# Performance work log

Hardware: AMD Instinct MI355X
Metric: run time of the kernel (lower is better)

Reference implementation:

```python
import jax, jax.numpy as jnp
import numpy as np

SR = 44100
D = SR * 30          # duration_samples = 1_323_000
N = 1024             # number of note events
L = 32768            # max note length in samples
W = 1024             # hann window length (module's window_length)
H = 8                # harmonics in the synth
K = 128              # FIR taps in the effect chain
LAT = 2              # time_latent_size


def setup_inputs() -> dict:
    key = jax.random.key(0)
    ks = jax.random.split(key, 10)
    freq_rad = jax.random.uniform(ks[0], (N,), jnp.float32, 0.01, 0.3)
    velocity = jax.random.uniform(ks[1], (N,), jnp.float32, 1.0, 127.0)
    starts = jax.random.randint(ks[2], (N,), 0, D - L, dtype=jnp.int32)
    lengths = jax.random.randint(ks[3], (N,), 2048, L + 1, dtype=jnp.int32)
    # time_embedder: Linear(1,32) -> ReLU -> Linear(32,LAT)
    w1 = jax.random.normal(ks[4], (1, 32), jnp.float32)
    b1 = jnp.zeros((32,), jnp.float32)
    w2 = jax.random.normal(ks[5], (32, LAT), jnp.float32) / jnp.sqrt(32.0)
    b2 = jnp.zeros((LAT,), jnp.float32)
    # synth amplitude MLP: [freq, vel, latent] (2+LAT) -> 64 -> H
    ws1 = jax.random.normal(ks[6], (2 + LAT, 64), jnp.float32)
    bs1 = jnp.zeros((64,), jnp.float32)
    ws2 = jax.random.normal(ks[7], (64, H), jnp.float32) / 8.0
    bs2 = jnp.zeros((H,), jnp.float32)
    # effect chain: causal FIR (OIW layout) + tanh
    fir = jax.random.normal(ks[8], (1, 1, K), jnp.float32) / K
    return dict(freq_rad=freq_rad, velocity=velocity,
                w1=w1, b1=b1, w2=w2, b2=b2,
                ws1=ws1, bs1=bs1, ws2=ws2, bs2=bs2, fir=fir,
                starts=starts, lengths=lengths, duration_samples=D)


def reference(freq_rad, velocity, w1, b1, w2, b2, ws1, bs1, ws2, bs2, fir,
              starts, lengths, duration_samples):
    Dn = int(duration_samples)
    t = jnp.arange(L, dtype=jnp.float32)            # [L]
    ti = jnp.arange(L, dtype=jnp.int32)             # [L]
    ends = starts + lengths
    # output_length = min(end, duration) - start, clipped to [0, L]
    out_len = jnp.clip(jnp.minimum(ends, Dn) - starts, 0, L)  # [N]
    # time latent: MLP on normalized start time
    nt = (starts.astype(jnp.float32) / Dn)[:, None]           # [N,1]
    lat = jax.nn.relu(nt @ w1 + b1) @ w2 + b2                  # [N,LAT]
    vel = (velocity / 127.0)[:, None]                          # [N,1]
    # harmonic amplitudes from tiny MLP (the 'synth')
    feat = jnp.concatenate([freq_rad[:, None], vel, lat], axis=-1)  # [N,2+LAT]
    amps = jax.nn.softplus(jax.nn.relu(feat @ ws1 + bs1) @ ws2 + bs2)  # [N,H]
    # additive synthesis; fixed small loop over harmonics, vectorized over [N,L]
    phase = freq_rad[:, None] * t[None, :]                     # [N,L]
    seg = jnp.zeros((N, L), jnp.float32)
    for hh in range(1, H + 1):
        seg = seg + amps[:, hh - 1:hh] * jnp.sin(hh * phase)
    seg = seg * vel
    # hann window (torch periodic) on the LAST W samples of each variable-length segment
    n = jnp.arange(W, dtype=jnp.float32)
    hann = 0.5 * (1.0 - jnp.cos(2.0 * jnp.pi * n / W))         # [W]
    wpos = ti[None, :] - (out_len[:, None] - W)                # [N,L]
    in_win = (wpos >= 0) & (wpos < W)
    factor = jnp.where(in_win, hann[jnp.clip(wpos, 0, W - 1)], 1.0)
    mask = (ti[None, :] < out_len[:, None]).astype(jnp.float32)  # zero past segment end
    seg = seg * factor * mask
    # effect chain: causal 128-tap FIR then tanh (masked so padding stays silent)
    y = jax.lax.conv_general_dilated(seg[:, None, :], fir,
                                     window_strides=(1,), padding=[(K - 1, 0)])
    seg = jnp.tanh(y[:, 0, :]) * mask                          # [N,L]
    # overlap-add: scatter each note into the output buffer
    idx = starts[:, None] + ti[None, :]                        # [N,L]
    valid = (ti[None, :] < out_len[:, None]) & (idx < Dn)
    contrib = jnp.where(valid, seg, 0.0)
    out = jnp.zeros((Dn,), jnp.float32).at[jnp.clip(idx, 0, Dn - 1).reshape(-1)].add(
        contrib.reshape(-1))
    return out
```

## Files before the change

### kernel.cpp

```cpp
#include <hip/hip_runtime.h>
#include <math.h>

#define LMAX  32768
#define WWIN  1024
#define KFIR  128
#define TO    1024
#define CPAD  1232
#define SYNTH 1152
#define ZPS   1148
#define SLOT  128

typedef _Float16 v8h __attribute__((ext_vector_type(8)));
typedef _Float16 v4h __attribute__((ext_vector_type(4)));
typedef float    v4f __attribute__((ext_vector_type(4)));
typedef float    v2f __attribute__((ext_vector_type(2)));

__device__ __forceinline__ float fast_tanh(float x) {
    float e = __builtin_amdgcn_exp2f(x * 2.8853900817779268f);
    return fmaf(-2.0f, __builtin_amdgcn_rcpf(e + 1.0f), 1.0f);
}

__global__ __launch_bounds__(256) void setup_notes_k(
    const float* __restrict__ freq_g, const float* __restrict__ velo_g,
    const float* __restrict__ w1,  const float* __restrict__ b1,
    const float* __restrict__ w2,  const float* __restrict__ b2,
    const float* __restrict__ ws1, const float* __restrict__ bs1,
    const float* __restrict__ ws2, const float* __restrict__ bs2,
    const int* __restrict__ starts, const int* __restrict__ lengths,
    float* __restrict__ npar, int* __restrict__ counts,
    unsigned short* __restrict__ lists,
    int Dn, int N, int n_tiles)
{
    __shared__ float s_w1[32], s_b1[32], s_w2[64], s_b2[2];
    __shared__ float s_ws1[256], s_bs1[64], s_ws2[512], s_bs2[8];
    const int tid = threadIdx.x;
    if (tid < 32) { s_w1[tid] = w1[tid]; s_b1[tid] = b1[tid]; }
    if (tid < 64) { s_w2[tid] = w2[tid]; s_bs1[tid] = bs1[tid]; }
    if (tid < 2)  s_b2[tid] = b2[tid];
    if (tid < 8)  s_bs2[tid] = bs2[tid];
    s_ws1[tid] = ws1[tid];
    s_ws2[tid] = ws2[tid];  s_ws2[tid + 256] = ws2[tid + 256];
    __syncthreads();

    const int j = blockIdx.x * 256 + tid;
    if (j >= N) return;

    int st  = starts[j];
    int len = lengths[j];
    int ol  = min(st + len, Dn) - st;
    ol = max(0, min(ol, LMAX));
    float v = velo_g[j] * (1.0f / 127.0f);
    float f = freq_g[j];
    float nt = (float)st / (float)Dn;
    float lat0 = s_b2[0], lat1 = s_b2[1];
    #pragma unroll
    for (int jj = 0; jj < 32; ++jj) {
        float h = fmaxf(fmaf(nt, s_w1[jj], s_b1[jj]), 0.0f);
        lat0 = fmaf(h, s_w2[jj * 2 + 0], lat0);
        lat1 = fmaf(h, s_w2[jj * 2 + 1], lat1);
    }
    float acc[8];
    #pragma unroll
    for (int h = 0; h < 8; ++h) acc[h] = s_bs2[h];
    #pragma unroll
    for (int jj = 0; jj < 64; ++jj) {
        float a = s_bs1[jj];
        a = fmaf(f,    s_ws1[0 * 64 + jj], a);
        a = fmaf(v,    s_ws1[1 * 64 + jj], a);
        a = fmaf(lat0, s_ws1[2 * 64 + jj], a);
        a = fmaf(lat1, s_ws1[3 * 64 + jj], a);
        a = fmaxf(a, 0.0f);
        #pragma unroll
        for (int h = 0; h < 8; ++h)
            acc[h] = fmaf(a, s_ws2[jj * 8 + h], acc[h]);
    }
    float* p = npar + (size_t)j * 12;
    p[0] = __int_as_float(st);
    p[1] = __int_as_float(ol);
    p[2] = f;
    p[3] = 0.0f;
    #pragma unroll
    for (int h = 0; h < 8; ++h) {
        float a = acc[h];
        float sp = fmaxf(a, 0.0f) + log1pf(expf(-fabsf(a)));
        p[4 + h] = sp * v;
    }

    if (ol > 0) {
        int t0 = st >> 10;
        int t1 = min((st + ol - 1) >> 10, n_tiles - 1);
        for (int t = t0; t <= t1; ++t) {
            int pos = atomicAdd(&counts[t], 1);
            if (pos < SLOT) lists[(size_t)t * SLOT + pos] = (unsigned short)j;
        }
    }
}

__global__ __launch_bounds__(1024) void sort_tiles_k(
    const int* __restrict__ counts, int* __restrict__ order, int n_tiles)
{
    __shared__ int hist[SLOT + 2];
    __shared__ int bstart[SLOT + 2];
    const int tid = threadIdx.x;
    if (tid < SLOT + 2) hist[tid] = 0;
    __syncthreads();
    for (int t = tid; t < n_tiles; t += 1024) {
        int k = min(counts[t], SLOT + 1);
        atomicAdd(&hist[k], 1);
    }
    __syncthreads();
    if (tid == 0) {
        int run = 0;
        for (int k = SLOT + 1; k >= 0; --k) { bstart[k] = run; run += hist[k]; }
    }
    __syncthreads();
    for (int t = tid; t < n_tiles; t += 1024) {
        int k = min(counts[t], SLOT + 1);
        int p = atomicAdd(&bstart[k], 1);
        order[p] = t;
    }
}

__global__ __launch_bounds__(256, 4) void synth_fused_k(
    const float* __restrict__ fir,
    const float* __restrict__ npar,
    const int* __restrict__ counts,
    const unsigned short* __restrict__ lists,
    const int* __restrict__ order,
    float* __restrict__ out, int Dn)
{
    __shared__ __align__(16) _Float16 segc[2][4][CPAD];
    __shared__ float fir_s[KFIR];
    __shared__ int   stl[SLOT], oll[SLOT];
    __shared__ float fl[SLOT];
    __shared__ __align__(16) float ampsl[SLOT][8];

    const int tid  = threadIdx.x;
    const int wid  = tid >> 6;
    const int lane = tid & 63;
    const int m    = lane & 15;
    const int quad = lane >> 4;
    const int tile = order[blockIdx.x];
    const int o0   = tile * TO;
    const int co   = 256 * wid;

    const int K = min(counts[tile], SLOT);

    if (tid < KFIR) fir_s[tid] = fir[tid];
    if (tid < K) {
        const int nid = (int)lists[(size_t)tile * SLOT + tid];
        const float4* pp = (const float4*)(npar + (size_t)nid * 12);
        float4 a = pp[0], b = pp[1], c = pp[2];
        stl[tid] = __float_as_int(a.x);
        oll[tid] = __float_as_int(a.y);
        fl[tid]  = a.z;
        *(float4*)&ampsl[tid][0] = b;
        *(float4*)&ampsl[tid][4] = c;
    }
    __syncthreads();

    v8h afrag[12];
    #pragma unroll
    for (int t = 0; t < 12; ++t) {
        v8h af;
        #pragma unroll
        for (int j = 0; j < 8; ++j) {
            int idx = 32 * t + 8 * quad + j - 16 * m;
            float fv = (idx >= 0 && idx < KFIR) ? fir_s[idx] : 0.0f;
            af[j] = (_Float16)fv;
        }
        afrag[t] = af;
    }
    for (int z = tid; z < 2 * 4 * (CPAD - ZPS); z += 256) {
        int b = z / (4 * (CPAD - ZPS));
        int r = z % (4 * (CPAD - ZPS));
        int S = r / (CPAD - ZPS), off = r % (CPAD - ZPS);
        segc[b][S][ZPS + off] = (_Float16)0.0f;
    }

    const _Float16* __restrict__ bb0 = &segc[0][m & 3][(m & ~3) + 8 * quad];
    const _Float16* __restrict__ bb1 = &segc[1][m & 3][(m & ~3) + 8 * quad];

    float accv[4] = {0.f, 0.f, 0.f, 0.f};
    const double inv2pi = 0.15915494309189535;
    int cur = 0;

    int stN = 0, olN = 0; float fN = 0.f;
    float4 amN0 = {}, amN1 = {};
    if (K > 0) {
        stN = stl[0]; olN = oll[0]; fN = fl[0];
        amN0 = *(const float4*)&ampsl[0][0];
        amN1 = *(const float4*)&ampsl[0][4];
    }

    const int nj = (wid == 0) ? 3 : 2;

    for (int kk = 0; kk < K; ++kk) {
        const int st = stN, ol = olN;
        const float f = fN;
        const float4 am0 = amN0, am1 = amN1;
        if (kk + 1 < K) {
            stN = stl[kk + 1]; olN = oll[kk + 1]; fN = fl[kk + 1];
            amN0 = *(const float4*)&ampsl[kk + 1][0];
            amN1 = *(const float4*)&ampsl[kk + 1][4];
        }

        const int base = o0 - st;
        if (base >= ol || base + TO <= 0) continue;

        const v2f A0v = {am0.x, am0.x}, A1v = {am0.y, am0.y};
        const v2f A2v = {am0.z, am0.z}, A3v = {am0.w, am0.w};
        const v2f A4v = {am1.x, am1.x}, A5v = {am1.y, am1.y};
        const v2f A6v = {am1.z, am1.z}, A7v = {am1.w, am1.w};
        const double fd = (double)f;
        const int wbase = ol - WWIN;

        const int tseed0 = base - 127 + lane + 128 * wid;
        double rev0 = fd * (double)tseed0 * inv2pi;
        double d64  = fd * 64.0 * inv2pi;
        double rev1 = rev0 + d64;
        double d512 = fd * 512.0 * inv2pi;
        float r0   = (float)(rev0 - floor(rev0));
        float r1   = (float)(rev1 - floor(rev1));
        float r512 = (float)(d512 - floor(d512));
        v2f s  = { __builtin_amdgcn_sinf(r0), __builtin_amdgcn_sinf(r1) };
        v2f cc = { __builtin_amdgcn_cosf(r0), __builtin_amdgcn_cosf(r1) };
        const float sd = __builtin_amdgcn_sinf(r512);
        const float cd = __builtin_amdgcn_cosf(r512);
        const v2f sdv = {sd, sd}, cdv = {cd, cd};

        const bool interior = (base >= 127) && (base + TO + 1 <= wbase);

        if (interior) {
            #pragma unroll
            for (int i = 0; i < 3; ++i) {
                if (i < nj) {
                    const int j = wid + 4 * i;
                    v2f tc = cc + cc;
                    v2f sA = s;
                    v2f sum = sA * A0v;
                    v2f sB = tc * sA;                                 sum = __builtin_elementwise_fma(A1v, sB, sum);
                    v2f sC = __builtin_elementwise_fma(tc, sB, -sA);  sum = __builtin_elementwise_fma(A2v, sC, sum);
                    v2f sD = __builtin_elementwise_fma(tc, sC, -sB);  sum = __builtin_elementwise_fma(A3v, sD, sum);
                    v2f sE = __builtin_elementwise_fma(tc, sD, -sC);  sum = __builtin_elementwise_fma(A4v, sE, sum);
                    v2f sF = __builtin_elementwise_fma(tc, sE, -sD);  sum = __builtin_elementwise_fma(A5v, sF, sum);
                    v2f sG = __builtin_elementwise_fma(tc, sF, -sE);  sum = __builtin_elementwise_fma(A6v, sG, sum);
                    v2f sH = __builtin_elementwise_fma(tc, sG, -sF);  sum = __builtin_elementwise_fma(A7v, sH, sum);
                    _Float16 h0 = (_Float16)sum.x;
                    _Float16 h1 = (_Float16)sum.y;
                    const int x0 = lane + 128 * j;
                    const int x1 = x0 + 64;
                    if (i == 0) {
                        #pragma unroll
                        for (int S = 0; S < 4; ++S)
                            if (x0 >= S) segc[cur][S][x0 - S] = h0;
                    } else {
                        #pragma unroll
                        for (int S = 0; S < 4; ++S)
                            segc[cur][S][x0 - S] = h0;
                    }
                    #pragma unroll
                    for (int S = 0; S < 4; ++S)
                        segc[cur][S][x1 - S] = h1;
                    v2f ns = __builtin_elementwise_fma(s, cdv, cc * sdv);
                    v2f nc = __builtin_elementwise_fma(cc, cdv, -(s * sdv));
                    s = ns; cc = nc;
                }
            }
        } else {
            #pragma unroll
            for (int i = 0; i < 3; ++i) {
                if (i < nj) {
                    const int j = wid + 4 * i;
                    const int t0 = tseed0 + 512 * i;
                    const int t1 = t0 + 64;
                    v2f tc = cc + cc;
                    v2f sA = s;
                    v2f sum = sA * A0v;
                    v2f sB = tc * sA;                                 sum = __builtin_elementwise_fma(A1v, sB, sum);
                    v2f sC = __builtin_elementwise_fma(tc, sB, -sA);  sum = __builtin_elementwise_fma(A2v, sC, sum);
                    v2f sD = __builtin_elementwise_fma(tc, sC, -sB);  sum = __builtin_elementwise_fma(A3v, sD, sum);
                    v2f sE = __builtin_elementwise_fma(tc, sD, -sC);  sum = __builtin_elementwise_fma(A4v, sE, sum);
                    v2f sF = __builtin_elementwise_fma(tc, sE, -sD);  sum = __builtin_elementwise_fma(A5v, sF, sum);
                    v2f sG = __builtin_elementwise_fma(tc, sF, -sE);  sum = __builtin_elementwise_fma(A6v, sG, sum);
                    v2f sH = __builtin_elementwise_fma(tc, sG, -sF);  sum = __builtin_elementwise_fma(A7v, sH, sum);
                    float v0 = 0.0f, v1 = 0.0f;
                    if (t0 >= 0 && t0 < ol) {
                        float factor = 1.0f;
                        int wpos = t0 - wbase;
                        if (wpos >= 0)
                            factor = 0.5f - 0.5f * __builtin_amdgcn_cosf((float)wpos * (1.0f / WWIN));
                        v0 = sum.x * factor;
                    }
                    if (t1 >= 0 && t1 < ol) {
                        float factor = 1.0f;
                        int wpos = t1 - wbase;
                        if (wpos >= 0)
                            factor = 0.5f - 0.5f * __builtin_amdgcn_cosf((float)wpos * (1.0f / WWIN));
                        v1 = sum.y * factor;
                    }
                    _Float16 h0 = (_Float16)v0;
                    _Float16 h1 = (_Float16)v1;
                    const int x0 = lane + 128 * j;
                    const int x1 = x0 + 64;
                    if (i == 0) {
                        #pragma unroll
                        for (int S = 0; S < 4; ++S)
                            if (x0 >= S) segc[cur][S][x0 - S] = h0;
                    } else {
                        #pragma unroll
                        for (int S = 0; S < 4; ++S)
                            segc[cur][S][x0 - S] = h0;
                    }
                    #pragma unroll
                    for (int S = 0; S < 4; ++S)
                        segc[cur][S][x1 - S] = h1;
                    v2f ns = __builtin_elementwise_fma(s, cdv, cc * sdv);
                    v2f nc = __builtin_elementwise_fma(cc, cdv, -(s * sdv));
                    s = ns; cc = nc;
                }
            }
        }

        __syncthreads();

        const _Float16* __restrict__ bb = cur ? bb1 : bb0;
        v4f CA0 = {0.f, 0.f, 0.f, 0.f};
        v4f CA1 = {0.f, 0.f, 0.f, 0.f};
        #pragma unroll
        for (int t = 0; t < 6; ++t) {
            v4h lo = *(const v4h*)(bb + co + 32 * t);
            v4h hi = *(const v4h*)(bb + co + 32 * t + 4);
            v8h bf = __builtin_shufflevector(lo, hi, 0, 1, 2, 3, 4, 5, 6, 7);
            CA0 = __builtin_amdgcn_mfma_f32_16x16x32_f16(afrag[t], bf, CA0, 0, 0, 0);
        }
        #pragma unroll
        for (int t = 6; t < 12; ++t) {
            v4h lo = *(const v4h*)(bb + co + 32 * t);
            v4h hi = *(const v4h*)(bb + co + 32 * t + 4);
            v8h bf = __builtin_shufflevector(lo, hi, 0, 1, 2, 3, 4, 5, 6, 7);
            CA1 = __builtin_amdgcn_mfma_f32_16x16x32_f16(afrag[t], bf, CA1, 0, 0, 0);
        }

        const int tb = base + co + 64 * quad + m;
        #pragma unroll
        for (int r = 0; r < 4; ++r) {
            float y = CA0[r] + CA1[r];
            if ((unsigned)(tb + 16 * r) < (unsigned)ol)
                accv[r] += fast_tanh(y);
        }

        cur ^= 1;
    }

    const int ob = o0 + co + 64 * quad + m;
    #pragma unroll
    for (int r = 0; r < 4; ++r)
        if (ob + 16 * r < Dn) out[ob + 16 * r] = accv[r];
}

extern "C" void kernel_launch(void* const* d_in, const int* in_sizes, int n_in,
                              void* d_out, int out_size, void* d_ws, size_t ws_size,
                              hipStream_t stream) {
    const float* freq    = (const float*)d_in[0];
    const float* velo    = (const float*)d_in[1];
    const float* w1      = (const float*)d_in[2];
    const float* b1      = (const float*)d_in[3];
    const float* w2      = (const float*)d_in[4];
    const float* b2      = (const float*)d_in[5];
    const float* ws1     = (const float*)d_in[6];
    const float* bs1     = (const float*)d_in[7];
    const float* ws2     = (const float*)d_in[8];
    const float* bs2     = (const float*)d_in[9];
    const float* fir     = (const float*)d_in[10];
    const int*   starts  = (const int*)d_in[11];
    const int*   lengths = (const int*)d_in[12];

    const int N  = in_sizes[0];
    const int Dn = out_size;
    float* out = (float*)d_out;

    const int n_tiles = (Dn + TO - 1) / TO;

    char* ws = (char*)d_ws;
    float* npar = (float*)ws;
    size_t off1 = ((size_t)N * 12 * sizeof(float) + 255) & ~(size_t)255;
    int* counts = (int*)(ws + off1);
    size_t off2 = off1 + (((size_t)n_tiles * sizeof(int) + 255) & ~(size_t)255);
    unsigned short* lists = (unsigned short*)(ws + off2);
    size_t off3 = off2 + (((size_t)n_tiles * SLOT * sizeof(unsigned short) + 255) & ~(size_t)255);
    int* order = (int*)(ws + off3);

    hipMemsetAsync(counts, 0, (size_t)n_tiles * sizeof(int), stream);
    setup_notes_k<<<(N + 255) / 256, 256, 0, stream>>>(
        freq, velo, w1, b1, w2, b2, ws1, bs1, ws2, bs2,
        starts, lengths, npar, counts, lists, Dn, N, n_tiles);
    sort_tiles_k<<<1, 1024, 0, stream>>>(counts, order, n_tiles);
    synth_fused_k<<<n_tiles, 256, 0, stream>>>(
        fir, npar, counts, lists, order, out, Dn);
}
```

Before: 153.9 us.

## Split output tiles into fixed-size note chunks with atomic accumulation

Each output tile's note list is now divided into work items of at most eight notes. Each item runs in its own block and adds its contribution to a zeroed output buffer with atomic adds, replacing the single block per tile that handled every overlapping note. This is meant to balance load across blocks, since tile note counts vary widely. The FIR MFMA fragments are also precomputed once into a global table instead of being built in every block. In exchange it adds an output memset, float atomics, redundant per-item FIR/tanh passes when a tile has several chunks, and a launch grid sized to the worst case, with excess blocks exiting early.

```diff
diff --git a/kernel.cpp b/kernel.cpp
--- a/kernel.cpp
+++ b/kernel.cpp
@@ -7,8 +7,8 @@
 #define TO    1024
 #define CPAD  1232
 #define SYNTH 1152
-#define ZPS   1148
 #define SLOT  128
+#define NCAP  8
 
 typedef _Float16 v8h __attribute__((ext_vector_type(8)));
 typedef _Float16 v4h __attribute__((ext_vector_type(4)));
@@ -26,9 +26,10 @@
     const float* __restrict__ w2,  const float* __restrict__ b2,
     const float* __restrict__ ws1, const float* __restrict__ bs1,
     const float* __restrict__ ws2, const float* __restrict__ bs2,
+    const float* __restrict__ fir,
     const int* __restrict__ starts, const int* __restrict__ lengths,
     float* __restrict__ npar, int* __restrict__ counts,
-    unsigned short* __restrict__ lists,
+    unsigned short* __restrict__ lists, _Float16* __restrict__ afrag_tab,
     int Dn, int N, int n_tiles)
 {
     __shared__ float s_w1[32], s_b1[32], s_w2[64], s_b2[2];
@@ -42,6 +43,21 @@
     s_ws2[tid] = ws2[tid];  s_ws2[tid + 256] = ws2[tid + 256];
     __syncthreads();
 
+    if (blockIdx.x == 0 && tid < 64) {
+        const int mm = tid & 15, qq = tid >> 4;
+        #pragma unroll
+        for (int t = 0; t < 12; ++t) {
+            v8h af;
+            #pragma unroll
+            for (int j = 0; j < 8; ++j) {
+                int idx = 32 * t + 8 * qq + j - 16 * mm;
+                float fv = (idx >= 0 && idx < KFIR) ? fir[idx] : 0.0f;
+                af[j] = (_Float16)fv;
+            }
+            *(v8h*)(afrag_tab + ((size_t)t * 64 + tid) * 8) = af;
+        }
+    }
+
     const int j = blockIdx.x * 256 + tid;
     if (j >= N) return;
 
@@ -96,59 +112,76 @@
     }
 }
 
-__global__ __launch_bounds__(1024) void sort_tiles_k(
-    const int* __restrict__ counts, int* __restrict__ order, int n_tiles)
+__global__ __launch_bounds__(1024) void build_items_k(
+    const int* __restrict__ counts, int* __restrict__ items,
+    int* __restrict__ n_items, int n_tiles)
 {
-    __shared__ int hist[SLOT + 2];
-    __shared__ int bstart[SLOT + 2];
+    __shared__ int hist[SLOT + 1];
+    __shared__ int bstart[SLOT + 1];
     const int tid = threadIdx.x;
-    if (tid < SLOT + 2) hist[tid] = 0;
+    if (tid < SLOT + 1) hist[tid] = 0;
     __syncthreads();
     for (int t = tid; t < n_tiles; t += 1024) {
-        int k = min(counts[t], SLOT + 1);
+        int k = min(counts[t], SLOT);
         atomicAdd(&hist[k], 1);
     }
     __syncthreads();
     if (tid == 0) {
         int run = 0;
-        for (int k = SLOT + 1; k >= 0; --k) { bstart[k] = run; run += hist[k]; }
+        for (int k = SLOT; k >= 1; --k) {
+            bstart[k] = run;
+            run += hist[k] * ((k + NCAP - 1) / NCAP);
+        }
+        n_items[0] = run;
     }
     __syncthreads();
     for (int t = tid; t < n_tiles; t += 1024) {
-        int k = min(counts[t], SLOT + 1);
-        int p = atomicAdd(&bstart[k], 1);
-        order[p] = t;
+        int k = min(counts[t], SLOT);
+        if (k == 0) continue;
+        int ni = (k + NCAP - 1) / NCAP;
+        int p = atomicAdd(&bstart[k], ni);
+        for (int i = 0; i < ni; ++i)
+            items[p + i] = t | ((i * NCAP) << 16);
     }
 }
 
 __global__ __launch_bounds__(256, 4) void synth_fused_k(
-    const float* __restrict__ fir,
+    const _Float16* __restrict__ afrag_tab,
     const float* __restrict__ npar,
     const int* __restrict__ counts,
     const unsigned short* __restrict__ lists,
-    const int* __restrict__ order,
+    const int* __restrict__ items,
+    const int* __restrict__ n_items,
     float* __restrict__ out, int Dn)
 {
     __shared__ __align__(16) _Float16 segc[2][4][CPAD];
-    __shared__ float fir_s[KFIR];
-    __shared__ int   stl[SLOT], oll[SLOT];
-    __shared__ float fl[SLOT];
-    __shared__ __align__(16) float ampsl[SLOT][8];
+    __shared__ int   stl[NCAP], oll[NCAP];
+    __shared__ float fl[NCAP];
+    __shared__ __align__(16) float ampsl[NCAP][8];
+
+    if ((int)blockIdx.x >= n_items[0]) return;
+
+    const int item = items[blockIdx.x];
+    const int tile = item & 0xffff;
+    const int koff = item >> 16;
 
     const int tid  = threadIdx.x;
     const int wid  = tid >> 6;
     const int lane = tid & 63;
     const int m    = lane & 15;
     const int quad = lane >> 4;
-    const int tile = order[blockIdx.x];
     const int o0   = tile * TO;
     const int co   = 256 * wid;
 
-    const int K = min(counts[tile], SLOT);
-
-    if (tid < KFIR) fir_s[tid] = fir[tid];
+    const int K = min(min(counts[tile], SLOT) - koff, NCAP);
+
+    v8h afrag[12];
+    #pragma unroll
+    for (int t = 0; t < 12; ++t)
+        afrag[t] = *(const v8h*)(afrag_tab + ((size_t)t * 64 + lane) * 8);
+
     if (tid < K) {
-        const int nid = (int)lists[(size_t)tile * SLOT + tid];
+        const int nid = (int)lists[(size_t)tile * SLOT + koff + tid];
         const float4* pp = (const float4*)(npar + (size_t)nid * 12);
         float4 a = pp[0], b = pp[1], c = pp[2];
         stl[tid] = __float_as_int(a.x);
@@ -157,26 +190,14 @@
         *(float4*)&ampsl[tid][0] = b;
         *(float4*)&ampsl[tid][4] = c;
     }
+
+    #pragma unroll
+    for (int b = 0; b < 2; ++b)
+        #pragma unroll
+        for (int S = 0; S < 4; ++S)
+            for (int i = SYNTH - S + tid; i < CPAD; i += 256)
+                segc[b][S][i] = (_Float16)0.0f;
     __syncthreads();
-
-    v8h afrag[12];
-    #pragma unroll
-    for (int t = 0; t < 12; ++t) {
-        v8h af;
-        #pragma unroll
-        for (int j = 0; j < 8; ++j) {
-            int idx = 32 * t + 8 * quad + j - 16 * m;
-            float fv = (idx >= 0 && idx < KFIR) ? fir_s[idx] : 0.0f;
-            af[j] = (_Float16)fv;
-        }
-        afrag[t] = af;
-    }
-    for (int z = tid; z < 2 * 4 * (CPAD - ZPS); z += 256) {
-        int b = z / (4 * (CPAD - ZPS));
-        int r = z % (4 * (CPAD - ZPS));
-        int S = r / (CPAD - ZPS), off = r % (CPAD - ZPS);
-        segc[b][S][ZPS + off] = (_Float16)0.0f;
-    }
 
     const _Float16* __restrict__ bb0 = &segc[0][m & 3][(m & ~3) + 8 * quad];
     const _Float16* __restrict__ bb1 = &segc[1][m & 3][(m & ~3) + 8 * quad];
@@ -356,7 +377,7 @@
     const int ob = o0 + co + 64 * quad + m;
     #pragma unroll
     for (int r = 0; r < 4; ++r)
-        if (ob + 16 * r < Dn) out[ob + 16 * r] = accv[r];
+        if (ob + 16 * r < Dn) atomicAdd(&out[ob + 16 * r], accv[r]);
 }
 
 extern "C" void kernel_launch(void* const* d_in, const int* in_sizes, int n_in,
@@ -381,6 +402,7 @@
     float* out = (float*)d_out;
 
     const int n_tiles = (Dn + TO - 1) / TO;
+    const int max_items = n_tiles + (N * (LMAX / TO + 1) + NCAP - 1) / NCAP;
 
     char* ws = (char*)d_ws;
     float* npar = (float*)ws;
@@ -389,13 +411,18 @@
     size_t off2 = off1 + (((size_t)n_tiles * sizeof(int) + 255) & ~(size_t)255);
     unsigned short* lists = (unsigned short*)(ws + off2);
     size_t off3 = off2 + (((size_t)n_tiles * SLOT * sizeof(unsigned short) + 255) & ~(size_t)255);
-    int* order = (int*)(ws + off3);
+    _Float16* afrag_tab = (_Float16*)(ws + off3);
+    size_t off4 = off3 + (((size_t)12 * 64 * 8 * sizeof(_Float16) + 255) & ~(size_t)255);
+    int* items = (int*)(ws + off4);
+    size_t off5 = off4 + (((size_t)max_items * sizeof(int) + 255) & ~(size_t)255);
+    int* n_items = (int*)(ws + off5);
 
     hipMemsetAsync(counts, 0, (size_t)n_tiles * sizeof(int), stream);
+    hipMemsetAsync(out, 0, (size_t)Dn * sizeof(float), stream);
     setup_notes_k<<<(N + 255) / 256, 256, 0, stream>>>(
-        freq, velo, w1, b1, w2, b2, ws1, bs1, ws2, bs2,
-        starts, lengths, npar, counts, lists, Dn, N, n_tiles);
-    sort_tiles_k<<<1, 1024, 0, stream>>>(counts, order, n_tiles);
-    synth_fused_k<<<n_tiles, 256, 0, stream>>>(
-        fir, npar, counts, lists, order, out, Dn);
+        freq, velo, w1, b1, w2, b2, ws1, bs1, ws2, bs2, fir,
+        starts, lengths, npar, counts, lists, afrag_tab, Dn, N, n_tiles);
+    build_items_k<<<1, 1024, 0, stream>>>(counts, items, n_items, n_tiles);
+    synth_fused_k<<<max_items, 256, 0, stream>>>(
+        afrag_tab, npar, counts, lists, items, n_items, out, Dn);
 }
```

Measured after the change: 162.7 us. 5.8% more time.
